# Kernel optimization log

Hardware: AMD Instinct MI355X
Metric: run time of the kernel (lower is better)

Reference implementation:

```python
import math
import jax, jax.numpy as jnp
import numpy as np

B, N, D, H, L = 8, 1024, 512, 8, 6
HD = D // H
FREQ = 256
K_LORENTZ = 1.0


def lorentz_projx(x, k=K_LORENTZ):
    # geoopt Lorentz.projx: x0 = sqrt(k + ||x_space||^2)
    space = x[..., 1:]
    x0 = jnp.sqrt(k + jnp.sum(space * space, axis=-1, keepdims=True))
    return jnp.concatenate([x0, space], axis=-1)


def layernorm(x, eps=1e-6):
    m = jnp.mean(x, axis=-1, keepdims=True)
    v = jnp.mean((x - m) ** 2, axis=-1, keepdims=True)
    return (x - m) / jnp.sqrt(v + eps)


def make_pe(n, d):
    pos = np.arange(n, dtype=np.float32)[:, None]
    div = np.exp(np.arange(0, d, 2, dtype=np.float32) * (-math.log(10000.0) / d))
    pe = np.zeros((n, d), dtype=np.float32)
    pe[:, 0::2] = np.sin(pos * div)
    pe[:, 1::2] = np.cos(pos * div)
    return jnp.asarray(pe)


def setup_inputs() -> dict:
    key = jax.random.key(0)
    ks = jax.random.split(key, 20)
    s = 0.02
    inp = {
        "t": jax.random.uniform(ks[0], (B,), jnp.float32) * 1000.0,
        "x": jax.random.normal(ks[1], (B, N, D), jnp.float32),
        "mask": jnp.ones((B, N), jnp.float32),
        "pe": make_pe(N, D),
        # timestep embedder MLP (weights stored [in,out])
        "tw1": jax.random.normal(ks[2], (FREQ, D), jnp.float32) * s,
        "tb1": jnp.zeros((D,), jnp.float32),
        "tw2": jax.random.normal(ks[3], (D, D), jnp.float32) * s,
        "tb2": jnp.zeros((D,), jnp.float32),
        # per-layer params stacked over L
        "Wq": jax.random.normal(ks[4], (L, D, D), jnp.float32) * s,
        "bq": jnp.zeros((L, D), jnp.float32),
        "Wk": jax.random.normal(ks[5], (L, D, D), jnp.float32) * s,
        "bk": jnp.zeros((L, D), jnp.float32),
        "Wv": jax.random.normal(ks[6], (L, D, D), jnp.float32) * s,
        "bv": jnp.zeros((L, D), jnp.float32),
        "W1": jax.random.normal(ks[7], (L, D, 4 * D), jnp.float32) * s,
        "b1": jnp.zeros((L, 4 * D), jnp.float32),
        "W2": jax.random.normal(ks[8], (L, 4 * D, D), jnp.float32) * s,
        "b2": jnp.zeros((L, D), jnp.float32),
        "Wada": jax.random.normal(ks[9], (L, D, 6 * D), jnp.float32) * s,
        "bada": jnp.zeros((L, 6 * D), jnp.float32),
    }
    return inp


def timestep_embedding(t, dim=FREQ, max_period=10000.0):
    half = dim // 2
    freqs = jnp.exp(-math.log(max_period) * jnp.arange(half, dtype=jnp.float32) / half)
    args = t[:, None] * freqs[None]
    return jnp.concatenate([jnp.cos(args), jnp.sin(args)], axis=-1)  # [B, dim]


def attention(h, mask, Wq, bq, Wk, bk, Wv, bv):
    # h: [B,N,D], mask: [B,N]
    q = (h @ Wq + bq).reshape(B, N, H, HD).transpose(0, 2, 1, 3)
    k = (h @ Wk + bk).reshape(B, N, H, HD).transpose(0, 2, 1, 3)
    v = (h @ Wv + bv).reshape(B, N, H, HD).transpose(0, 2, 1, 3)
    scores = jnp.einsum("bhqd,bhkd->bhqk", q, k) / math.sqrt(HD)
    # faithful quirk: valid positions get +1 added, invalid get -10000
    mm = jnp.einsum("bi,bj->bij", mask, mask)[:, None]  # [B,1,N,N]
    mm = jnp.where(mm == 0, -10000.0, mm)
    scores = scores + mm
    probs = jax.nn.softmax(scores, axis=-1)
    ctx = jnp.einsum("bhqk,bhkd->bhqd", probs, v)
    return ctx.transpose(0, 2, 1, 3).reshape(B, N, D)


def reference(t, x, mask, pe, tw1, tb1, tw2, tb2, Wq, bq, Wk, bk, Wv, bv,
              W1, b1, W2, b2, Wada, bada):
    # z = x + PositionalEncoding(x) = 2*x + pe
    z = x + (x + pe[None])
    # timestep embedder
    c = timestep_embedding(t) @ tw1 + tb1
    c = jax.nn.silu(c) @ tw2 + tb2  # [B, D]
    for i in range(L):
        ada = jax.nn.silu(c) @ Wada[i] + bada[i]  # [B, 6D]
        sh_msa, sc_msa, g_msa, sh_mlp, sc_mlp, g_mlp = jnp.split(ada, 6, axis=-1)
        h = layernorm(z) * (1.0 + sc_msa[:, None]) + sh_msa[:, None]
        z = z + g_msa[:, None] * attention(h, mask, Wq[i], bq[i], Wk[i], bk[i], Wv[i], bv[i])
        z = lorentz_projx(z)
        h = layernorm(z) * (1.0 + sc_mlp[:, None]) + sh_mlp[:, None]
        m = jax.nn.gelu(h @ W1[i] + b1[i], approximate=True) @ W2[i] + b2[i]
        z = z + g_mlp[:, None] * m
        z = lorentz_projx(z)
    z = lorentz_projx(z)
    return jnp.where(mask[:, :, None] != 0, z, 0.0)
```

## Files before the change

kernel.cpp:

```cpp
#include <hip/hip_runtime.h>
#include <hip/hip_bf16.h>
#include <math.h>

#define NTOK 1024
#define DMODEL 512
#define NHEAD 8
#define HDIM 64
#define BATCH 8
#define NLAYER 6
#define ROWS (BATCH*NTOK)
#define QKVSTR 1536
#define LOG2E 1.44269504f

typedef __attribute__((ext_vector_type(8))) short bf16x8;
typedef __attribute__((ext_vector_type(4))) float f32x4;
typedef unsigned short ushort_t;


__device__ __forceinline__ float silu_f(float x) { return x / (1.f + expf(-x)); }

__device__ __forceinline__ float gelu_tanh_f(float x) {
    float x3 = x * x * x;
    float y2 = 1.5957691216057308f * (x + 0.044715f * x3);
    float e = __builtin_amdgcn_exp2f(-y2 * LOG2E);
    return x / (1.f + e);
}

__device__ __forceinline__ unsigned short f2bf(float x) {
    __hip_bfloat16 b = __float2bfloat16(x);
    return *reinterpret_cast<unsigned short*>(&b);
}

__device__ __forceinline__ float bf2f(unsigned short u) {
    union { float f; unsigned v; } c;
    c.v = (unsigned)u << 16;
    return c.f;
}

__device__ __forceinline__ float wave_sum(float v) {
    #pragma unroll
    for (int o = 1; o < 64; o <<= 1) v += __shfl_xor(v, o);
    return v;
}


__global__ __launch_bounds__(256) void init_z_kernel(const float* __restrict__ x,
                                                     const float* __restrict__ pe,
                                                     float* __restrict__ z) {
    int i = blockIdx.x * 256 + threadIdx.x;
    const int C4 = DMODEL / 4;
    int row = i / C4;
    int col4 = i - row * C4;
    int n = row & (NTOK - 1);
    float4 xv = ((const float4*)x)[i];
    float4 pv = ((const float4*)pe)[n * C4 + col4];
    float4 o;
    o.x = 2.f * xv.x + pv.x;
    o.y = 2.f * xv.y + pv.y;
    o.z = 2.f * xv.z + pv.z;
    o.w = 2.f * xv.w + pv.w;
    ((float4*)z)[i] = o;
}

__global__ void temb_kernel(const float* __restrict__ t, float* __restrict__ temb) {
    int b = blockIdx.x;
    int j = threadIdx.x;
    float f = expf(-9.210340371976184f * (float)j / 128.f);
    float a = t[b] * f;
    temb[b * 256 + j] = cosf(a);
    temb[b * 256 + 128 + j] = sinf(a);
}

__global__ __launch_bounds__(256) void skinny_part(const float* __restrict__ A,
                                                   const float* __restrict__ W,
                                                   float* __restrict__ part,
                                                   int K, int N, int NL) {
    __shared__ float Als[8][128];
    const int l = blockIdx.z;
    const int n = blockIdx.x * 256 + threadIdx.x;
    const int kc = blockIdx.y;
    const int kbase = kc * 128;
    for (int i = threadIdx.x; i < 8 * 128; i += 256) {
        int b = i >> 7, k = i & 127;
        Als[b][k] = A[b * K + kbase + k];
    }
    __syncthreads();
    float acc[8] = {};
    const float* wp = W + (size_t)l * K * N + (size_t)kbase * N + n;
    for (int k = 0; k < 128; k += 4) {
        float w0 = wp[0];
        float w1 = wp[N];
        float w2 = wp[2 * N];
        float w3 = wp[3 * N];
        wp += 4 * (size_t)N;
        #pragma unroll
        for (int b = 0; b < 8; b++)
            acc[b] += Als[b][k] * w0 + Als[b][k + 1] * w1 + Als[b][k + 2] * w2 + Als[b][k + 3] * w3;
    }
    #pragma unroll
    for (int b = 0; b < 8; b++)
        part[((size_t)kc * 8 + b) * NL + (size_t)l * N + n] = acc[b];
}

template<int ACT>
__global__ __launch_bounds__(256) void skinny_reduce(const float* __restrict__ part,
                                                     const float* __restrict__ bias,
                                                     float* __restrict__ out,
                                                     int KC, int N, int NL) {
    int i = blockIdx.x * 256 + threadIdx.x;
    if (i >= 8 * NL) return;
    int b = i / NL, n = i - b * NL;
    float s = bias[n];
    for (int kc = 0; kc < KC; kc++) s += part[((size_t)kc * 8 + b) * NL + n];
    if (ACT == 1) s = silu_f(s);
    int l = n / N, nl = n - l * N;
    out[((size_t)l * 8 + b) * N + nl] = s;
}

__global__ __launch_bounds__(256) void transp_all(const float* __restrict__ Wq,
                                                  const float* __restrict__ Wk,
                                                  const float* __restrict__ Wv,
                                                  const float* __restrict__ W1,
                                                  const float* __restrict__ W2,
                                                  ushort_t* __restrict__ wqkv_t,
                                                  ushort_t* __restrict__ w1_t,
                                                  ushort_t* __restrict__ w2_t) {
    __shared__ float tile[32][33];
    int blk = blockIdx.x;
    const float* src; ushort_t* dst; int K, N, k0, n0;
    if (blk < 768) {
        int zz = blk >> 8, rem = blk & 255;
        k0 = (rem >> 4) * 32; n0 = (rem & 15) * 32;
        src = zz == 0 ? Wq : (zz == 1 ? Wk : Wv);
        dst = wqkv_t + zz * 512 * 512;
        K = 512; N = 512;
    } else if (blk < 1792) {
        int rem = blk - 768;
        n0 = (rem & 63) * 32; k0 = (rem >> 6) * 32;
        src = W1; dst = w1_t; K = 512; N = 2048;
    } else {
        int rem = blk - 1792;
        n0 = (rem & 15) * 32; k0 = (rem >> 4) * 32;
        src = W2; dst = w2_t; K = 2048; N = 512;
    }
    int c = threadIdx.x & 31, r8 = threadIdx.x >> 5;
    #pragma unroll
    for (int i = 0; i < 4; i++) {
        int r = r8 + i * 8;
        tile[r][c] = src[(size_t)(k0 + r) * N + n0 + c];
    }
    __syncthreads();
    #pragma unroll
    for (int i = 0; i < 4; i++) {
        int rr = r8 + i * 8;
        dst[(size_t)(n0 + rr) * K + k0 + c] = f2bf(tile[c][rr]);
    }
}

__global__ void pack_bias(const float* __restrict__ bq, const float* __restrict__ bk,
                          const float* __restrict__ bv, float* __restrict__ bqkv) {
    int idx = blockIdx.x * 256 + threadIdx.x;
    if (idx >= NLAYER * QKVSTR) return;
    int l = idx / QKVSTR, n = idx - l * QKVSTR;
    float v = (n < 512) ? bq[l * 512 + n] : (n < 1024) ? bk[l * 512 + n - 512] : bv[l * 512 + n - 1024];
    bqkv[idx] = v;
}

template<int ACT, int OUTBF, int QPRESCALE>
__global__ __launch_bounds__(256) void mfma_gemm(const ushort_t* __restrict__ A,
                                                 const ushort_t* __restrict__ Bt,
                                                 const float* __restrict__ bias,
                                                 void* __restrict__ Cout,
                                                 int M, int N, int K) {
    __shared__ ushort_t smem[4 * 128 * 64];
    const int tid = threadIdx.x;
    const int lane = tid & 63, wv = tid >> 6;
    const int wm = (wv >> 1) * 64, wn = (wv & 1) * 64;
    const int lrow = lane & 15, lk = lane >> 4;
    const int m0 = blockIdx.x * 128, n0 = blockIdx.y * 128;
    const int srow = lane >> 3;
    const int qp = lane & 7;
    const int ql = qp ^ srow;

    f32x4 acc[4][4];
    #pragma unroll
    for (int i = 0; i < 4; i++)
        #pragma unroll
        for (int j = 0; j < 4; j++) {
            f32x4 zz = {0.f, 0.f, 0.f, 0.f};
            acc[i][j] = zz;
        }

    const int nK = K >> 6;

    auto STAGE = [&](int p, int ks) {
        const int k0 = ks << 6;
        ushort_t* Ad = smem + p * 8192;
        ushort_t* Bd = smem + 16384 + p * 8192;
        #pragma unroll
        for (int it = 0; it < 4; it++) {
            int chunk = wv * 4 + it;
            int row = chunk * 8 + srow;
            const ushort_t* srcA = A + (size_t)(m0 + row) * K + k0 + ql * 8;
            const ushort_t* srcB = Bt + (size_t)(n0 + row) * K + k0 + ql * 8;
            __builtin_amdgcn_global_load_lds((const __attribute__((address_space(1))) void*)srcA,
                                             (__attribute__((address_space(3))) void*)(Ad + chunk * 512),
                                             16, 0, 0);
            __builtin_amdgcn_global_load_lds((const __attribute__((address_space(1))) void*)srcB,
                                             (__attribute__((address_space(3))) void*)(Bd + chunk * 512),
                                             16, 0, 0);
        }
    };

    STAGE(0, 0);
    int cur = 0;
    for (int ks = 0; ks < nK; ks++) {
        if (ks + 1 < nK) {
            STAGE(cur ^ 1, ks + 1);
            asm volatile("s_waitcnt vmcnt(8)" ::: "memory");
        } else {
            asm volatile("s_waitcnt vmcnt(0)" ::: "memory");
        }
        __builtin_amdgcn_s_barrier();
        asm volatile("" ::: "memory");

        const ushort_t* Ab = smem + cur * 8192;
        const ushort_t* Bb = smem + 16384 + cur * 8192;
        #pragma unroll
        for (int kk = 0; kk < 2; kk++) {
            bf16x8 af[4], bfr[4];
            #pragma unroll
            for (int f = 0; f < 4; f++) {
                int ar = wm + f * 16 + lrow;
                af[f] = *(const bf16x8*)(Ab + ar * 64 + (((kk * 4 + lk) ^ (ar & 7)) << 3));
                int br = wn + f * 16 + lrow;
                bfr[f] = *(const bf16x8*)(Bb + br * 64 + (((kk * 4 + lk) ^ (br & 7)) << 3));
            }
            #pragma unroll
            for (int i = 0; i < 4; i++)
                #pragma unroll
                for (int j = 0; j < 4; j++)
                    acc[i][j] = __builtin_amdgcn_mfma_f32_16x16x32_bf16(af[i], bfr[j], acc[i][j], 0, 0, 0);
        }
        asm volatile("" ::: "memory");
        __builtin_amdgcn_s_barrier();
        cur ^= 1;
    }

    if (OUTBF) {
        __syncthreads();
        #pragma unroll
        for (int j = 0; j < 4; j++) {
            int coll = wn + j * 16 + lrow;
            float bcol = bias[n0 + coll];
            #pragma unroll
            for (int i = 0; i < 4; i++) {
                #pragma unroll
                for (int r = 0; r < 4; r++) {
                    int rowl = wm + i * 16 + lk * 4 + r;
                    float v = acc[i][j][r] + bcol;
                    if (ACT == 1) v = gelu_tanh_f(v);
                    if (QPRESCALE && (n0 + coll) < 512) v *= 0.125f * LOG2E;
                    smem[rowl * 136 + coll] = f2bf(v);
                }
            }
        }
        __syncthreads();
        ushort_t* Co = (ushort_t*)Cout;
        #pragma unroll
        for (int pass = 0; pass < 8; pass++) {
            int rowl = pass * 16 + (tid >> 4);
            int cseg = (tid & 15) * 8;
            uint4 vv = *(const uint4*)(smem + rowl * 136 + cseg);
            *(uint4*)(Co + (size_t)(m0 + rowl) * N + n0 + cseg) = vv;
        }
    } else {
        #pragma unroll
        for (int j = 0; j < 4; j++) {
            int col = n0 + wn + j * 16 + lrow;
            float bcol = bias[col];
            #pragma unroll
            for (int i = 0; i < 4; i++)
                #pragma unroll
                for (int r = 0; r < 4; r++) {
                    int row = m0 + wm + i * 16 + lk * 4 + r;
                    float v = acc[i][j][r] + bcol;
                    if (ACT == 1) v = gelu_tanh_f(v);
                    ((float*)Cout)[(size_t)row * N + col] = v;
                }
        }
    }
}


__global__ __launch_bounds__(256) void ln_mod_kernel(const float* __restrict__ z,
                                                     const float* __restrict__ ada,
                                                     ushort_t* __restrict__ out,
                                                     int sh_off, int sc_off) {
    int lane = threadIdx.x & 63;
    int row = blockIdx.x * 4 + (threadIdx.x >> 6);
    int b = row >> 10;
    const float4* zr = (const float4*)(z + (size_t)row * DMODEL);
    float4 va = zr[lane * 2], vb = zr[lane * 2 + 1];
    float s = va.x + va.y + va.z + va.w + vb.x + vb.y + vb.z + vb.w;
    float mean = wave_sum(s) * (1.f / DMODEL);
    float d0 = va.x - mean, d1 = va.y - mean, d2 = va.z - mean, d3 = va.w - mean;
    float d4 = vb.x - mean, d5 = vb.y - mean, d6 = vb.z - mean, d7 = vb.w - mean;
    float ssq = d0*d0 + d1*d1 + d2*d2 + d3*d3 + d4*d4 + d5*d5 + d6*d6 + d7*d7;
    float rstd = rsqrtf(wave_sum(ssq) * (1.f / DMODEL) + 1e-6f);
    const float* ab = ada + b * (6 * DMODEL);
    const float4* scp = (const float4*)(ab + sc_off);
    const float4* shp = (const float4*)(ab + sh_off);
    float4 sca = scp[lane * 2], scb = scp[lane * 2 + 1];
    float4 sha = shp[lane * 2], shb = shp[lane * 2 + 1];
    uint4 pk;
    pk.x = (unsigned)f2bf(d0 * rstd * (1.f + sca.x) + sha.x) |
           ((unsigned)f2bf(d1 * rstd * (1.f + sca.y) + sha.y) << 16);
    pk.y = (unsigned)f2bf(d2 * rstd * (1.f + sca.z) + sha.z) |
           ((unsigned)f2bf(d3 * rstd * (1.f + sca.w) + sha.w) << 16);
    pk.z = (unsigned)f2bf(d4 * rstd * (1.f + scb.x) + shb.x) |
           ((unsigned)f2bf(d5 * rstd * (1.f + scb.y) + shb.y) << 16);
    pk.w = (unsigned)f2bf(d6 * rstd * (1.f + scb.z) + shb.z) |
           ((unsigned)f2bf(d7 * rstd * (1.f + scb.w) + shb.w) << 16);
    ((uint4*)(out + (size_t)row * DMODEL))[lane] = pk;
}

__global__ __launch_bounds__(256) void resid_ln_kernel(float* __restrict__ z,
                                                       const ushort_t* __restrict__ add,
                                                       const float* __restrict__ adaG, int g_off,
                                                       const float* __restrict__ adaLN, int sh_off, int sc_off,
                                                       ushort_t* __restrict__ out) {
    int lane = threadIdx.x & 63;
    int row = blockIdx.x * 4 + (threadIdx.x >> 6);
    int b = row >> 10;
    float4* zr = (float4*)(z + (size_t)row * DMODEL);
    float4 va = zr[lane * 2], vb = zr[lane * 2 + 1];
    uint4 a4 = ((const uint4*)(add + (size_t)row * DMODEL))[lane];
    const float4* gp = (const float4*)(adaG + b * (6 * DMODEL) + g_off);
    float4 ga = gp[lane * 2], gb = gp[lane * 2 + 1];
    const ushort_t* e = (const ushort_t*)&a4;
    va.x += ga.x * bf2f(e[0]); va.y += ga.y * bf2f(e[1]);
    va.z += ga.z * bf2f(e[2]); va.w += ga.w * bf2f(e[3]);
    vb.x += gb.x * bf2f(e[4]); vb.y += gb.y * bf2f(e[5]);
    vb.z += gb.z * bf2f(e[6]); vb.w += gb.w * bf2f(e[7]);
    float ssq = va.x*va.x + va.y*va.y + va.z*va.z + va.w*va.w
              + vb.x*vb.x + vb.y*vb.y + vb.z*vb.z + vb.w*vb.w;
    if (lane == 0) ssq -= va.x * va.x;
    float tot = wave_sum(ssq);
    if (lane == 0) va.x = sqrtf(1.f + tot);
    zr[lane * 2] = va; zr[lane * 2 + 1] = vb;
    float s = va.x + va.y + va.z + va.w + vb.x + vb.y + vb.z + vb.w;
    float mean = wave_sum(s) * (1.f / DMODEL);
    float d0 = va.x - mean, d1 = va.y - mean, d2 = va.z - mean, d3 = va.w - mean;
    float d4 = vb.x - mean, d5 = vb.y - mean, d6 = vb.z - mean, d7 = vb.w - mean;
    float sq2 = d0*d0 + d1*d1 + d2*d2 + d3*d3 + d4*d4 + d5*d5 + d6*d6 + d7*d7;
    float rstd = rsqrtf(wave_sum(sq2) * (1.f / DMODEL) + 1e-6f);
    const float* ab = adaLN + b * (6 * DMODEL);
    const float4* scp = (const float4*)(ab + sc_off);
    const float4* shp = (const float4*)(ab + sh_off);
    float4 sca = scp[lane * 2], scb = scp[lane * 2 + 1];
    float4 sha = shp[lane * 2], shb = shp[lane * 2 + 1];
    uint4 pk;
    pk.x = (unsigned)f2bf(d0 * rstd * (1.f + sca.x) + sha.x) |
           ((unsigned)f2bf(d1 * rstd * (1.f + sca.y) + sha.y) << 16);
    pk.y = (unsigned)f2bf(d2 * rstd * (1.f + sca.z) + sha.z) |
           ((unsigned)f2bf(d3 * rstd * (1.f + sca.w) + sha.w) << 16);
    pk.z = (unsigned)f2bf(d4 * rstd * (1.f + scb.x) + shb.x) |
           ((unsigned)f2bf(d5 * rstd * (1.f + scb.y) + shb.y) << 16);
    pk.w = (unsigned)f2bf(d6 * rstd * (1.f + scb.z) + shb.z) |
           ((unsigned)f2bf(d7 * rstd * (1.f + scb.w) + shb.w) << 16);
    ((uint4*)(out + (size_t)row * DMODEL))[lane] = pk;
}

__global__ __launch_bounds__(256) void resid_final_kernel(const float* __restrict__ z,
                                                          const ushort_t* __restrict__ add,
                                                          const float* __restrict__ adaG, int g_off,
                                                          const float* __restrict__ mask,
                                                          float* __restrict__ out) {
    int lane = threadIdx.x & 63;
    int row = blockIdx.x * 4 + (threadIdx.x >> 6);
    int b = row >> 10;
    const float4* zr = (const float4*)(z + (size_t)row * DMODEL);
    float4 va = zr[lane * 2], vb = zr[lane * 2 + 1];
    uint4 a4 = ((const uint4*)(add + (size_t)row * DMODEL))[lane];
    const float4* gp = (const float4*)(adaG + b * (6 * DMODEL) + g_off);
    float4 ga = gp[lane * 2], gb = gp[lane * 2 + 1];
    const ushort_t* e = (const ushort_t*)&a4;
    va.x += ga.x * bf2f(e[0]); va.y += ga.y * bf2f(e[1]);
    va.z += ga.z * bf2f(e[2]); va.w += ga.w * bf2f(e[3]);
    vb.x += gb.x * bf2f(e[4]); vb.y += gb.y * bf2f(e[5]);
    vb.z += gb.z * bf2f(e[6]); vb.w += gb.w * bf2f(e[7]);
    float ssq = va.x*va.x + va.y*va.y + va.z*va.z + va.w*va.w
              + vb.x*vb.x + vb.y*vb.y + vb.z*vb.z + vb.w*vb.w;
    if (lane == 0) ssq -= va.x * va.x;
    float tot = wave_sum(ssq);
    if (lane == 0) va.x = sqrtf(1.f + tot);
    float m = mask[row];
    if (m == 0.f) {
        va.x = va.y = va.z = va.w = 0.f;
        vb.x = vb.y = vb.z = vb.w = 0.f;
    }
    float4* orow = (float4*)(out + (size_t)row * DMODEL);
    orow[lane * 2] = va; orow[lane * 2 + 1] = vb;
}

__global__ __launch_bounds__(256) void flash_attn_mfma(const ushort_t* __restrict__ qkv,
                                                       const float* __restrict__ mask,
                                                       ushort_t* __restrict__ ctx) {
    __shared__ ushort_t Kls[64 * 64];
    __shared__ ushort_t Vt[64 * 64];
    __shared__ ushort_t Pls[4][16 * 64];
    __shared__ float Mall[NTOK];

    const int tid = threadIdx.x;
    const int lane = tid & 63, w = tid >> 6;
    const int c = lane & 15, g = lane >> 4;
    const int bh = blockIdx.x;
    const int q0 = blockIdx.y * 64;
    const int b = bh >> 3, h = bh & 7;

    const ushort_t* qptr = qkv + (size_t)(b * NTOK + q0 + w * 16 + c) * QKVSTR + h * HDIM + g * 8;
    bf16x8 aq0 = *(const bf16x8*)(qptr);
    bf16x8 aq1 = *(const bf16x8*)(qptr + 32);

    const float mqL = mask[b * NTOK + q0 + w * 16 + c] * LOG2E;

    #pragma unroll
    for (int i = 0; i < 4; i++) Mall[tid + i * 256] = mask[b * NTOK + tid + i * 256];

    f32x4 o[4];
    #pragma unroll
    for (int j = 0; j < 4; j++) { f32x4 zz = {0.f,0.f,0.f,0.f}; o[j] = zz; }
    float l_run = 0.f;

    const int srow = lane >> 3, qp = lane & 7, ql = qp ^ srow;
    const int kp = tid & 31, dg = tid >> 5;

    char* Pw = (char*)&Pls[w][0];
    const int cswz = (c & 7) << 4;

    for (int kt = 0; kt < NTOK / 64; kt++) {
        const int k0 = kt * 64;
        __syncthreads();
        #pragma unroll
        for (int it = 0; it < 2; it++) {
            int chunk = w * 2 + it;
            int row = chunk * 8 + srow;
            const ushort_t* src = qkv + (size_t)(b * NTOK + k0 + row) * QKVSTR + 512 + h * HDIM + ql * 8;
            __builtin_amdgcn_global_load_lds((const __attribute__((address_space(1))) void*)src,
                                             (__attribute__((address_space(3))) void*)(Kls + chunk * 512),
                                             16, 0, 0);
        }
        {
            const ushort_t* v0 = qkv + (size_t)(b * NTOK + k0 + 2 * kp) * QKVSTR + 1024 + h * HDIM + dg * 8;
            uint4 r0 = *(const uint4*)v0;
            uint4 r1 = *(const uint4*)(v0 + QKVSTR);
            const ushort_t* e0 = (const ushort_t*)&r0;
            const ushort_t* e1 = (const ushort_t*)&r1;
            unsigned* VtU = (unsigned*)Vt;
            #pragma unroll
            for (int i = 0; i < 8; i++) {
                int d = dg * 8 + i;
                unsigned pk = (unsigned)e0[i] | ((unsigned)e1[i] << 16);
                VtU[d * 32 + (((kp >> 2) ^ (d & 7)) << 2) + (kp & 3)] = pk;
            }
        }
        __syncthreads();

        f32x4 s[4];
        #pragma unroll
        for (int j = 0; j < 4; j++) { f32x4 zz = {0.f,0.f,0.f,0.f}; s[j] = zz; }
        __builtin_amdgcn_s_setprio(1);
        #pragma unroll
        for (int j = 0; j < 4; j++) {
            int row = j * 16 + c;
            bf16x8 ak0 = *(const bf16x8*)(Kls + row * 64 + ((g ^ (row & 7)) << 3));
            bf16x8 ak1 = *(const bf16x8*)(Kls + row * 64 + (((4 + g) ^ (row & 7)) << 3));
            s[j] = __builtin_amdgcn_mfma_f32_16x16x32_bf16(ak0, aq0, s[j], 0, 0, 0);
            s[j] = __builtin_amdgcn_mfma_f32_16x16x32_bf16(ak1, aq1, s[j], 0, 0, 0);
        }
        __builtin_amdgcn_s_setprio(0);

        #pragma unroll
        for (int j = 0; j < 4; j++) {
            float4 mk4 = *(const float4*)&Mall[k0 + j * 16 + 4 * g];
            const float* mkp = (const float*)&mk4;
            unsigned u[4];
            #pragma unroll
            for (int r = 0; r < 4; r++) {
                float v = mqL * mkp[r];
                float sv = s[j][r] + (v == 0.f ? -14427.0f : v);
                float p = exp2f(sv);
                l_run += p;
                u[r] = __float_as_uint(p);
            }
            uint2 pk2;
            pk2.x = (u[0] >> 16) | (u[1] & 0xffff0000u);
            pk2.y = (u[2] >> 16) | (u[3] & 0xffff0000u);
            *(uint2*)(Pw + c * 128 + ((j * 32 + g * 8) ^ cswz)) = pk2;
        }

        __builtin_amdgcn_s_setprio(1);
        #pragma unroll
        for (int kk = 0; kk < 2; kk++) {
            bf16x8 pa = *(const bf16x8*)(Pw + c * 128 + ((kk * 64 + g * 16) ^ cswz));
            #pragma unroll
            for (int j = 0; j < 4; j++) {
                int vr = j * 16 + c;
                bf16x8 bv = *(const bf16x8*)(Vt + vr * 64 + (((kk * 4 + g) ^ (vr & 7)) << 3));
                o[j] = __builtin_amdgcn_mfma_f32_16x16x32_bf16(pa, bv, o[j], 0, 0, 0);
            }
        }
        __builtin_amdgcn_s_setprio(0);
    }

    l_run += __shfl_xor(l_run, 16);
    l_run += __shfl_xor(l_run, 32);

    float invr[4];
    #pragma unroll
    for (int r = 0; r < 4; r++) invr[r] = 1.f / __shfl(l_run, (g << 4) + 4 * g + r);
    #pragma unroll
    for (int r = 0; r < 4; r++) {
        size_t row = (size_t)(b * NTOK + q0 + w * 16 + 4 * g + r) * DMODEL + h * HDIM;
        #pragma unroll
        for (int j = 0; j < 4; j++)
            ctx[row + j * 16 + c] = f2bf(o[j][r] * invr[r]);
    }
}


extern "C" void kernel_launch(void* const* d_in, const int* in_sizes, int n_in,
                              void* d_out, int out_size, void* d_ws, size_t ws_size,
                              hipStream_t stream) {
    const float* t    = (const float*)d_in[0];
    const float* x    = (const float*)d_in[1];
    const float* mask = (const float*)d_in[2];
    const float* pe   = (const float*)d_in[3];
    const float* tw1  = (const float*)d_in[4];
    const float* tb1  = (const float*)d_in[5];
    const float* tw2  = (const float*)d_in[6];
    const float* tb2  = (const float*)d_in[7];
    const float* Wq   = (const float*)d_in[8];
    const float* bq   = (const float*)d_in[9];
    const float* Wk   = (const float*)d_in[10];
    const float* bk   = (const float*)d_in[11];
    const float* Wv   = (const float*)d_in[12];
    const float* bv   = (const float*)d_in[13];
    const float* W1   = (const float*)d_in[14];
    const float* b1   = (const float*)d_in[15];
    const float* W2   = (const float*)d_in[16];
    const float* b2   = (const float*)d_in[17];
    const float* Wada = (const float*)d_in[18];
    const float* bada = (const float*)d_in[19];
    float* out = (float*)d_out;

    float* z      = (float*)d_ws;
    ushort_t* cxb = (ushort_t*)(z + (size_t)ROWS * DMODEL);
    ushort_t* qkv = cxb + (size_t)ROWS * DMODEL;
    ushort_t* mid = qkv;
    ushort_t* hb  = qkv + (size_t)ROWS * 2048;
    ushort_t* wqkv_t = hb + (size_t)ROWS * DMODEL;
    ushort_t* w1_t   = wqkv_t + 1536 * 512;
    ushort_t* w2_t   = w1_t + 2048 * 512;
    float* bqkv  = (float*)(w2_t + 512 * 2048);
    float* temb  = bqkv + NLAYER * QKVSTR;
    float* cmid  = temb + BATCH * 256;
    float* scs   = cmid + BATCH * DMODEL;
    float* part  = scs + BATCH * DMODEL;
    float* ada_all = part + 4 * 8 * (NLAYER * 3072);

    init_z_kernel<<<ROWS * DMODEL / 4 / 256, 256, 0, stream>>>(x, pe, z);
    temb_kernel<<<BATCH, 128, 0, stream>>>(t, temb);
    pack_bias<<<(NLAYER * QKVSTR + 255) / 256, 256, 0, stream>>>(bq, bk, bv, bqkv);

    skinny_part<<<dim3(2, 2, 1), 256, 0, stream>>>(temb, tw1, part, 256, 512, 512);
    skinny_reduce<1><<<16, 256, 0, stream>>>(part, tb1, cmid, 2, 512, 512);
    skinny_part<<<dim3(2, 4, 1), 256, 0, stream>>>(cmid, tw2, part, 512, 512, 512);
    skinny_reduce<1><<<16, 256, 0, stream>>>(part, tb2, scs, 4, 512, 512);
    skinny_part<<<dim3(12, 4, NLAYER), 256, 0, stream>>>(scs, Wada, part, 512, 3072, NLAYER * 3072);
    skinny_reduce<0><<<(8 * NLAYER * 3072 + 255) / 256, 256, 0, stream>>>(
        part, bada, ada_all, 4, 3072, NLAYER * 3072);

    dim3 gqkv(ROWS / 128, QKVSTR / 128);
    dim3 gmlp1(ROWS / 128, 2048 / 128);
    dim3 gmlp2(ROWS / 128, DMODEL / 128);
    dim3 ga(BATCH * NHEAD, NTOK / 64);

    ln_mod_kernel<<<ROWS / 4, 256, 0, stream>>>(z, ada_all, hb, 0, 512);

    for (int i = 0; i < NLAYER; i++) {
        const float* ada = ada_all + (size_t)i * 8 * 3072;

        transp_all<<<2816, 256, 0, stream>>>(Wq + (size_t)i * 512 * 512,
                                             Wk + (size_t)i * 512 * 512,
                                             Wv + (size_t)i * 512 * 512,
                                             W1 + (size_t)i * 512 * 2048,
                                             W2 + (size_t)i * 2048 * 512,
                                             wqkv_t, w1_t, w2_t);

        mfma_gemm<0, 1, 1><<<gqkv, 256, 0, stream>>>(hb, wqkv_t, bqkv + i * QKVSTR, qkv,
                                                     ROWS, QKVSTR, DMODEL);

        flash_attn_mfma<<<ga, 256, 0, stream>>>(qkv, mask, cxb);

        resid_ln_kernel<<<ROWS / 4, 256, 0, stream>>>(z, cxb, ada, 2 * DMODEL,
                                                      ada, 3 * DMODEL, 4 * DMODEL, hb);

        mfma_gemm<1, 1, 0><<<gmlp1, 256, 0, stream>>>(hb, w1_t, b1 + (size_t)i * 4 * DMODEL, mid,
                                                      ROWS, 4 * DMODEL, DMODEL);
        mfma_gemm<0, 1, 0><<<gmlp2, 256, 0, stream>>>(mid, w2_t, b2 + (size_t)i * DMODEL, cxb,
                                                      ROWS, DMODEL, 4 * DMODEL);

        if (i < NLAYER - 1) {
            const float* adan = ada_all + (size_t)(i + 1) * 8 * 3072;
            resid_ln_kernel<<<ROWS / 4, 256, 0, stream>>>(z, cxb, ada, 5 * DMODEL,
                                                          adan, 0, 512, hb);
        } else {
            resid_final_kernel<<<ROWS / 4, 256, 0, stream>>>(z, cxb, ada, 5 * DMODEL, mask, out);
        }
    }
}
```

Baseline: 955.5 us.

## Split-K the MLP down-projection and widen attention blocks to 128 queries

The second MLP GEMM (K=2048, only 256 tiles) is split into two K halves. Each half writes its own bf16 partial buffer, and the residual/LN kernel sums the two partials plus the bias. Flash attention now uses 512 threads covering 128 queries per block, which halves K/V staging per query, and the P conversion switches from truncation to rounded bf16. This raises GEMM occupancy and cuts attention load traffic, at the cost of an extra partial-buffer round trip and more bf16 rounding in the split sum.

```diff
diff --git a/kernel.cpp b/kernel.cpp
--- a/kernel.cpp
+++ b/kernel.cpp
@@ -69,6 +69,10 @@
     float a = t[b] * f;
     temb[b * 256 + j] = cosf(a);
     temb[b * 256 + 128 + j] = sinf(a);
+}
+
+__global__ void zero512(float* __restrict__ p) {
+    p[blockIdx.x * 256 + threadIdx.x] = 0.f;
 }
 
 __global__ __launch_bounds__(256) void skinny_part(const float* __restrict__ A,
@@ -166,7 +170,7 @@
     bqkv[idx] = v;
 }
 
-template<int ACT, int OUTBF, int QPRESCALE>
+template<int ACT, int OUTBF, int QPRESCALE, int SPLITK>
 __global__ __launch_bounds__(256) void mfma_gemm(const ushort_t* __restrict__ A,
                                                  const ushort_t* __restrict__ Bt,
                                                  const float* __restrict__ bias,
@@ -182,6 +186,15 @@
     const int qp = lane & 7;
     const int ql = qp ^ srow;
 
+    int Keff = K;
+    if (SPLITK) {
+        Keff = K >> 1;
+        const size_t koff = (size_t)blockIdx.z * Keff;
+        A += koff;
+        Bt += koff;
+        Cout = (void*)((ushort_t*)Cout + (size_t)blockIdx.z * M * N);
+    }
+
     f32x4 acc[4][4];
     #pragma unroll
     for (int i = 0; i < 4; i++)
@@ -191,7 +204,7 @@
             acc[i][j] = zz;
         }
 
-    const int nK = K >> 6;
+    const int nK = Keff >> 6;
 
     auto STAGE = [&](int p, int ks) {
         const int k0 = ks << 6;
@@ -325,8 +338,11 @@
     ((uint4*)(out + (size_t)row * DMODEL))[lane] = pk;
 }
 
+template<int TWO>
 __global__ __launch_bounds__(256) void resid_ln_kernel(float* __restrict__ z,
                                                        const ushort_t* __restrict__ add,
+                                                       const ushort_t* __restrict__ add2,
+                                                       const float* __restrict__ abias,
                                                        const float* __restrict__ adaG, int g_off,
                                                        const float* __restrict__ adaLN, int sh_off, int sc_off,
                                                        ushort_t* __restrict__ out) {
@@ -339,10 +355,23 @@
     const float4* gp = (const float4*)(adaG + b * (6 * DMODEL) + g_off);
     float4 ga = gp[lane * 2], gb = gp[lane * 2 + 1];
     const ushort_t* e = (const ushort_t*)&a4;
-    va.x += ga.x * bf2f(e[0]); va.y += ga.y * bf2f(e[1]);
-    va.z += ga.z * bf2f(e[2]); va.w += ga.w * bf2f(e[3]);
-    vb.x += gb.x * bf2f(e[4]); vb.y += gb.y * bf2f(e[5]);
-    vb.z += gb.z * bf2f(e[6]); vb.w += gb.w * bf2f(e[7]);
+    float av[8];
+    #pragma unroll
+    for (int i = 0; i < 8; i++) av[i] = bf2f(e[i]);
+    if (TWO) {
+        uint4 a42 = ((const uint4*)(add2 + (size_t)row * DMODEL))[lane];
+        const ushort_t* e2 = (const ushort_t*)&a42;
+        float4 ba = ((const float4*)abias)[lane * 2];
+        float4 bb = ((const float4*)abias)[lane * 2 + 1];
+        av[0] += bf2f(e2[0]) + ba.x; av[1] += bf2f(e2[1]) + ba.y;
+        av[2] += bf2f(e2[2]) + ba.z; av[3] += bf2f(e2[3]) + ba.w;
+        av[4] += bf2f(e2[4]) + bb.x; av[5] += bf2f(e2[5]) + bb.y;
+        av[6] += bf2f(e2[6]) + bb.z; av[7] += bf2f(e2[7]) + bb.w;
+    }
+    va.x += ga.x * av[0]; va.y += ga.y * av[1];
+    va.z += ga.z * av[2]; va.w += ga.w * av[3];
+    vb.x += gb.x * av[4]; vb.y += gb.y * av[5];
+    vb.z += gb.z * av[6]; vb.w += gb.w * av[7];
     float ssq = va.x*va.x + va.y*va.y + va.z*va.z + va.w*va.w
               + vb.x*vb.x + vb.y*vb.y + vb.z*vb.z + vb.w*vb.w;
     if (lane == 0) ssq -= va.x * va.x;
@@ -374,6 +403,8 @@
 
 __global__ __launch_bounds__(256) void resid_final_kernel(const float* __restrict__ z,
                                                           const ushort_t* __restrict__ add,
+                                                          const ushort_t* __restrict__ add2,
+                                                          const float* __restrict__ abias,
                                                           const float* __restrict__ adaG, int g_off,
                                                           const float* __restrict__ mask,
                                                           float* __restrict__ out) {
@@ -383,13 +414,21 @@
     const float4* zr = (const float4*)(z + (size_t)row * DMODEL);
     float4 va = zr[lane * 2], vb = zr[lane * 2 + 1];
     uint4 a4 = ((const uint4*)(add + (size_t)row * DMODEL))[lane];
+    uint4 a42 = ((const uint4*)(add2 + (size_t)row * DMODEL))[lane];
     const float4* gp = (const float4*)(adaG + b * (6 * DMODEL) + g_off);
     float4 ga = gp[lane * 2], gb = gp[lane * 2 + 1];
     const ushort_t* e = (const ushort_t*)&a4;
-    va.x += ga.x * bf2f(e[0]); va.y += ga.y * bf2f(e[1]);
-    va.z += ga.z * bf2f(e[2]); va.w += ga.w * bf2f(e[3]);
-    vb.x += gb.x * bf2f(e[4]); vb.y += gb.y * bf2f(e[5]);
-    vb.z += gb.z * bf2f(e[6]); vb.w += gb.w * bf2f(e[7]);
+    const ushort_t* e2 = (const ushort_t*)&a42;
+    float4 ba = ((const float4*)abias)[lane * 2];
+    float4 bb = ((const float4*)abias)[lane * 2 + 1];
+    va.x += ga.x * (bf2f(e[0]) + bf2f(e2[0]) + ba.x);
+    va.y += ga.y * (bf2f(e[1]) + bf2f(e2[1]) + ba.y);
+    va.z += ga.z * (bf2f(e[2]) + bf2f(e2[2]) + ba.z);
+    va.w += ga.w * (bf2f(e[3]) + bf2f(e2[3]) + ba.w);
+    vb.x += gb.x * (bf2f(e[4]) + bf2f(e2[4]) + bb.x);
+    vb.y += gb.y * (bf2f(e[5]) + bf2f(e2[5]) + bb.y);
+    vb.z += gb.z * (bf2f(e[6]) + bf2f(e2[6]) + bb.z);
+    vb.w += gb.w * (bf2f(e[7]) + bf2f(e2[7]) + bb.w);
     float ssq = va.x*va.x + va.y*va.y + va.z*va.z + va.w*va.w
               + vb.x*vb.x + vb.y*vb.y + vb.z*vb.z + vb.w*vb.w;
     if (lane == 0) ssq -= va.x * va.x;
@@ -404,29 +443,29 @@
     orow[lane * 2] = va; orow[lane * 2 + 1] = vb;
 }
 
-__global__ __launch_bounds__(256) void flash_attn_mfma(const ushort_t* __restrict__ qkv,
+__global__ __launch_bounds__(512) void flash_attn_mfma(const ushort_t* __restrict__ qkv,
                                                        const float* __restrict__ mask,
                                                        ushort_t* __restrict__ ctx) {
     __shared__ ushort_t Kls[64 * 64];
     __shared__ ushort_t Vt[64 * 64];
-    __shared__ ushort_t Pls[4][16 * 64];
+    __shared__ ushort_t Pls[8][16 * 64];
     __shared__ float Mall[NTOK];
 
     const int tid = threadIdx.x;
     const int lane = tid & 63, w = tid >> 6;
     const int c = lane & 15, g = lane >> 4;
     const int bh = blockIdx.x;
-    const int q0 = blockIdx.y * 64;
+    const int q0 = blockIdx.y * 128;
     const int b = bh >> 3, h = bh & 7;
 
     const ushort_t* qptr = qkv + (size_t)(b * NTOK + q0 + w * 16 + c) * QKVSTR + h * HDIM + g * 8;
     bf16x8 aq0 = *(const bf16x8*)(qptr);
     bf16x8 aq1 = *(const bf16x8*)(qptr + 32);
 
-    const float mqL = mask[b * NTOK + q0 + w * 16 + c] * LOG2E;
-
-    #pragma unroll
-    for (int i = 0; i < 4; i++) Mall[tid + i * 256] = mask[b * NTOK + tid + i * 256];
+    const float mq = mask[b * NTOK + q0 + w * 16 + c];
+
+    #pragma unroll
+    for (int i = 0; i < 2; i++) Mall[tid + i * 512] = mask[b * NTOK + tid + i * 512];
 
     f32x4 o[4];
     #pragma unroll
@@ -442,25 +481,23 @@
     for (int kt = 0; kt < NTOK / 64; kt++) {
         const int k0 = kt * 64;
         __syncthreads();
-        #pragma unroll
-        for (int it = 0; it < 2; it++) {
-            int chunk = w * 2 + it;
-            int row = chunk * 8 + srow;
+        {
+            int row = w * 8 + srow;
             const ushort_t* src = qkv + (size_t)(b * NTOK + k0 + row) * QKVSTR + 512 + h * HDIM + ql * 8;
             __builtin_amdgcn_global_load_lds((const __attribute__((address_space(1))) void*)src,
-                                             (__attribute__((address_space(3))) void*)(Kls + chunk * 512),
+                                             (__attribute__((address_space(3))) void*)(Kls + w * 512),
                                              16, 0, 0);
         }
         {
-            const ushort_t* v0 = qkv + (size_t)(b * NTOK + k0 + 2 * kp) * QKVSTR + 1024 + h * HDIM + dg * 8;
-            uint4 r0 = *(const uint4*)v0;
-            uint4 r1 = *(const uint4*)(v0 + QKVSTR);
+            const ushort_t* v0 = qkv + (size_t)(b * NTOK + k0 + 2 * kp) * QKVSTR + 1024 + h * HDIM + dg * 4;
+            uint2 r0 = *(const uint2*)v0;
+            uint2 r1 = *(const uint2*)(v0 + QKVSTR);
             const ushort_t* e0 = (const ushort_t*)&r0;
             const ushort_t* e1 = (const ushort_t*)&r1;
             unsigned* VtU = (unsigned*)Vt;
             #pragma unroll
-            for (int i = 0; i < 8; i++) {
-                int d = dg * 8 + i;
+            for (int i = 0; i < 4; i++) {
+                int d = dg * 4 + i;
                 unsigned pk = (unsigned)e0[i] | ((unsigned)e1[i] << 16);
                 VtU[d * 32 + (((kp >> 2) ^ (d & 7)) << 2) + (kp & 3)] = pk;
             }
@@ -485,18 +522,17 @@
         for (int j = 0; j < 4; j++) {
             float4 mk4 = *(const float4*)&Mall[k0 + j * 16 + 4 * g];
             const float* mkp = (const float*)&mk4;
-            unsigned u[4];
+            float p[4];
             #pragma unroll
             for (int r = 0; r < 4; r++) {
-                float v = mqL * mkp[r];
-                float sv = s[j][r] + (v == 0.f ? -14427.0f : v);
-                float p = exp2f(sv);
-                l_run += p;
-                u[r] = __float_as_uint(p);
+                float mm = mq * mkp[r];
+                float sv = s[j][r] + (mm == 0.f ? -14427.0f : mm * LOG2E);
+                p[r] = exp2f(sv);
+                l_run += p[r];
             }
             uint2 pk2;
-            pk2.x = (u[0] >> 16) | (u[1] & 0xffff0000u);
-            pk2.y = (u[2] >> 16) | (u[3] & 0xffff0000u);
+            pk2.x = (unsigned)f2bf(p[0]) | ((unsigned)f2bf(p[1]) << 16);
+            pk2.y = (unsigned)f2bf(p[2]) | ((unsigned)f2bf(p[3]) << 16);
             *(uint2*)(Pw + c * 128 + ((j * 32 + g * 8) ^ cswz)) = pk2;
         }
 
@@ -557,14 +593,16 @@
 
     float* z      = (float*)d_ws;
     ushort_t* cxb = (ushort_t*)(z + (size_t)ROWS * DMODEL);
-    ushort_t* qkv = cxb + (size_t)ROWS * DMODEL;
+    ushort_t* cxb2 = cxb + (size_t)ROWS * DMODEL;
+    ushort_t* qkv = cxb2 + (size_t)ROWS * DMODEL;
     ushort_t* mid = qkv;
     ushort_t* hb  = qkv + (size_t)ROWS * 2048;
     ushort_t* wqkv_t = hb + (size_t)ROWS * DMODEL;
     ushort_t* w1_t   = wqkv_t + 1536 * 512;
     ushort_t* w2_t   = w1_t + 2048 * 512;
     float* bqkv  = (float*)(w2_t + 512 * 2048);
-    float* temb  = bqkv + NLAYER * QKVSTR;
+    float* fzero = bqkv + NLAYER * QKVSTR;
+    float* temb  = fzero + 512;
     float* cmid  = temb + BATCH * 256;
     float* scs   = cmid + BATCH * DMODEL;
     float* part  = scs + BATCH * DMODEL;
@@ -573,6 +611,7 @@
     init_z_kernel<<<ROWS * DMODEL / 4 / 256, 256, 0, stream>>>(x, pe, z);
     temb_kernel<<<BATCH, 128, 0, stream>>>(t, temb);
     pack_bias<<<(NLAYER * QKVSTR + 255) / 256, 256, 0, stream>>>(bq, bk, bv, bqkv);
+    zero512<<<2, 256, 0, stream>>>(fzero);
 
     skinny_part<<<dim3(2, 2, 1), 256, 0, stream>>>(temb, tw1, part, 256, 512, 512);
     skinny_reduce<1><<<16, 256, 0, stream>>>(part, tb1, cmid, 2, 512, 512);
@@ -584,8 +623,8 @@
 
     dim3 gqkv(ROWS / 128, QKVSTR / 128);
     dim3 gmlp1(ROWS / 128, 2048 / 128);
-    dim3 gmlp2(ROWS / 128, DMODEL / 128);
-    dim3 ga(BATCH * NHEAD, NTOK / 64);
+    dim3 gmlp2(ROWS / 128, DMODEL / 128, 2);
+    dim3 ga(BATCH * NHEAD, NTOK / 128);
 
     ln_mod_kernel<<<ROWS / 4, 256, 0, stream>>>(z, ada_all, hb, 0, 512);
 
@@ -599,25 +638,28 @@
                                              W2 + (size_t)i * 2048 * 512,
                                              wqkv_t, w1_t, w2_t);
 
-        mfma_gemm<0, 1, 1><<<gqkv, 256, 0, stream>>>(hb, wqkv_t, bqkv + i * QKVSTR, qkv,
-                                                     ROWS, QKVSTR, DMODEL);
-
-        flash_attn_mfma<<<ga, 256, 0, stream>>>(qkv, mask, cxb);
-
-        resid_ln_kernel<<<ROWS / 4, 256, 0, stream>>>(z, cxb, ada, 2 * DMODEL,
-                                                      ada, 3 * DMODEL, 4 * DMODEL, hb);
-
-        mfma_gemm<1, 1, 0><<<gmlp1, 256, 0, stream>>>(hb, w1_t, b1 + (size_t)i * 4 * DMODEL, mid,
-                                                      ROWS, 4 * DMODEL, DMODEL);
-        mfma_gemm<0, 1, 0><<<gmlp2, 256, 0, stream>>>(mid, w2_t, b2 + (size_t)i * DMODEL, cxb,
-                                                      ROWS, DMODEL, 4 * DMODEL);
+        mfma_gemm<0, 1, 1, 0><<<gqkv, 256, 0, stream>>>(hb, wqkv_t, bqkv + i * QKVSTR, qkv,
+                                                        ROWS, QKVSTR, DMODEL);
+
+        flash_attn_mfma<<<ga, 512, 0, stream>>>(qkv, mask, cxb);
+
+        resid_ln_kernel<0><<<ROWS / 4, 256, 0, stream>>>(z, cxb, nullptr, nullptr,
+                                                         ada, 2 * DMODEL,
+                                                         ada, 3 * DMODEL, 4 * DMODEL, hb);
+
+        mfma_gemm<1, 1, 0, 0><<<gmlp1, 256, 0, stream>>>(hb, w1_t, b1 + (size_t)i * 4 * DMODEL, mid,
+                                                         ROWS, 4 * DMODEL, DMODEL);
+        mfma_gemm<0, 1, 0, 1><<<gmlp2, 256, 0, stream>>>(mid, w2_t, fzero, cxb,
+                                                         ROWS, DMODEL, 4 * DMODEL);
 
         if (i < NLAYER - 1) {
             const float* adan = ada_all + (size_t)(i + 1) * 8 * 3072;
-            resid_ln_kernel<<<ROWS / 4, 256, 0, stream>>>(z, cxb, ada, 5 * DMODEL,
-                                                          adan, 0, 512, hb);
+            resid_ln_kernel<1><<<ROWS / 4, 256, 0, stream>>>(z, cxb, cxb2, b2 + (size_t)i * DMODEL,
+                                                             ada, 5 * DMODEL,
+                                                             adan, 0, 512, hb);
         } else {
-            resid_final_kernel<<<ROWS / 4, 256, 0, stream>>>(z, cxb, ada, 5 * DMODEL, mask, out);
-        }
-    }
-}
+            resid_final_kernel<<<ROWS / 4, 256, 0, stream>>>(z, cxb, cxb2, b2 + (size_t)i * DMODEL,
+                                                             ada, 5 * DMODEL, mask, out);
+        }
+    }
+}
```

After: 913.9 us. -4.4%, faster.
